# Kernel tuning notes

Measured on AMD Instinct MI355X. Metric: run time of the kernel, lower is better.

The kernel has to match this reference:

```python
import jax, jax.numpy as jnp
import numpy as np
from jax import lax

B, S, D, H = 8, 1024, 512, 8
K = 25  # moving-average kernel
EPS = 1e-6


def setup_inputs() -> dict:
    key = jax.random.key(0)
    ks = jax.random.split(key, 8)

    def dense_w(k, din, dout):
        return (jax.random.normal(k, (din, dout), jnp.float32) / np.sqrt(din).astype(np.float32))

    return {
        "x": jax.random.normal(ks[0], (B, S, D), jnp.float32),
        "wq": dense_w(ks[1], D, D), "bq": jnp.zeros((D,), jnp.float32),
        "wk": dense_w(ks[2], D, D), "bk": jnp.zeros((D,), jnp.float32),
        "wv": dense_w(ks[3], D, D), "bv": jnp.zeros((D,), jnp.float32),
        "wo": dense_w(ks[4], D, D), "bo": jnp.zeros((D,), jnp.float32),
        "w1": dense_w(ks[5], D, 4 * D), "b1": jnp.zeros((4 * D,), jnp.float32),
        "w2": dense_w(ks[6], 4 * D, D), "b2": jnp.zeros((D,), jnp.float32),
        "g1": jnp.ones((D,), jnp.float32), "be1": jnp.zeros((D,), jnp.float32),
        "g2": jnp.ones((D,), jnp.float32), "be2": jnp.zeros((D,), jnp.float32),
        "g3": jnp.ones((D,), jnp.float32), "be3": jnp.zeros((D,), jnp.float32),
        "num_heads": H,
    }


def _moving_avg(x):
    # TF AveragePooling1D(pool=K, stride=1, padding='same'): divisor excludes padding.
    s = lax.reduce_window(x, 0.0, lax.add, (1, K, 1), (1, 1, 1), 'SAME')
    cnt = lax.reduce_window(jnp.ones((1, x.shape[1], 1), x.dtype), 0.0, lax.add,
                            (1, K, 1), (1, 1, 1), 'SAME')
    return s / cnt


def _layernorm(x, g, b):
    m = jnp.mean(x, -1, keepdims=True)
    v = jnp.var(x, -1, keepdims=True)
    return (x - m) * jax.lax.rsqrt(v + EPS) * g + b


def _auto_correlation(x, wq, bq, wk, bk, wv, bv, wo, bo, num_heads):
    b, s, d = x.shape
    dp = d // num_heads
    def split_heads(t):
        return t.reshape(b, s, num_heads, dp).transpose(0, 2, 1, 3)  # [B,H,S,dp]
    q = split_heads(x @ wq + bq)
    k = split_heads(x @ wk + bk)
    v = split_heads(x @ wv + bv)
    # Faithful to source: rfft over innermost (depth) axis, fft_length = 2*S.
    qf = jnp.fft.rfft(q, n=2 * s, axis=-1)
    kf = jnp.fft.rfft(k, n=2 * s, axis=-1)
    corr = jnp.fft.irfft(qf * jnp.conj(kf), n=2 * s, axis=-1)[..., :s]  # [B,H,S,S]
    scale = 1.0 / np.sqrt(dp).astype(np.float32)
    attn = jax.nn.softmax(scale * corr, axis=-1)
    out = jnp.einsum('bhst,bhtd->bhsd', attn, v)
    out = out.transpose(0, 2, 1, 3).reshape(b, s, d)
    return out @ wo + bo


def reference(x, wq, bq, wk, bk, wv, bv, wo, bo, w1, b1, w2, b2,
              g1, be1, g2, be2, g3, be3, num_heads):
    trend_init = _moving_avg(x)
    seasonal_init = x - trend_init
    attn_out = _auto_correlation(seasonal_init, wq, bq, wk, bk, wv, bv, wo, bo, num_heads)
    out1 = _layernorm(attn_out + seasonal_init, g1, be1)
    ffn = jax.nn.relu(out1 @ w1 + b1) @ w2 + b2
    seasonal_out = _layernorm(out1 + ffn, g2, be2) + seasonal_init
    trend2 = _moving_avg(seasonal_out)
    seasonal_final = seasonal_out - trend2
    x_out = seasonal_final + (trend2 + trend_init)
    return _layernorm(x_out, g3, be3)
```

## Files before the change

### kernel.cpp

```cpp
#include <hip/hip_runtime.h>
#include <cstdint>


typedef float f32x4 __attribute__((ext_vector_type(4)));
typedef __bf16 bf16x8 __attribute__((ext_vector_type(8)));
typedef _Float16 h2t __attribute__((ext_vector_type(2)));
typedef unsigned short u16;
typedef unsigned int u32;
typedef u32 u32x4 __attribute__((ext_vector_type(4)));

__device__ __forceinline__ u16 f2bf(float f) {
  unsigned int u = __float_as_uint(f);
  u = (u + 0x7FFFu + ((u >> 16) & 1u)) >> 16;
  return (u16)u;
}

__device__ __forceinline__ float bf2f(u16 b) { return __uint_as_float((u32)b << 16); }

__device__ __forceinline__ u16 f2h(float f) {
  _Float16 hv = (_Float16)f;
  u16 b;
  __builtin_memcpy(&b, &hv, 2);
  return b;
}

__device__ __forceinline__ float dot2h(u32 qp, u32 kp_, float c) {
#if __has_builtin(__builtin_amdgcn_fdot2)
  return __builtin_amdgcn_fdot2(__builtin_bit_cast(h2t, qp),
                                __builtin_bit_cast(h2t, kp_), c, false);
#else
  h2t q = __builtin_bit_cast(h2t, qp), k = __builtin_bit_cast(h2t, kp_);
  c = fmaf((float)q.x, (float)k.x, c);
  return fmaf((float)q.y, (float)k.y, c);
#endif
}

__device__ __forceinline__ void gload_lds16(const void* g, void* l) {
  __builtin_amdgcn_global_load_lds((__attribute__((address_space(1))) void*)g,
                                   (__attribute__((address_space(3))) void*)l,
                                   16, 0, 0);
}

__global__ __launch_bounds__(256) void movavg_kernel(
    const float* __restrict__ x, float* __restrict__ seas,
    u16* __restrict__ seas_bf, u16* __restrict__ a64, float* __restrict__ srow) {
  int blk = blockIdx.x;
  int sc = blk & 127, b = blk >> 7;
  int d = threadIdx.x * 2;
  const float* xb = x + (size_t)b * 1024 * 512 + d;
  int s0 = sc * 8;
  int lo = max(s0 - 12, 0), hi = min(s0 + 12, 1023);
  float sx = 0.f, sy = 0.f;
  for (int j = lo; j <= hi; ++j) {
    float2 v = *(const float2*)&xb[(size_t)j * 512];
    sx += v.x;
    sy += v.y;
  }
  float ax = 0.f, ay = 0.f;
#pragma unroll
  for (int s = s0; s < s0 + 8; ++s) {
    int l2 = max(s - 12, 0), h2 = min(s + 12, 1023);
    float invc = 1.f / (float)(h2 - l2 + 1);
    float2 xv = *(const float2*)&xb[(size_t)s * 512];
    float sex = xv.x - sx * invc;
    float sey = xv.y - sy * invc;
    size_t idx = (size_t)(b * 1024 + s) * 512 + d;
    u32 pk = (u32)f2bf(sex) | ((u32)f2bf(sey) << 16);
    *(float2*)&seas[idx] = make_float2(sex, sey);
    *(u32*)&seas_bf[idx] = pk;
    if (s < 64) *(u32*)&a64[(size_t)(b * 64 + s) * 512 + d] = pk;
    ax += sex;
    ay += sey;
    if (s - 12 >= 0) {
      float2 v = *(const float2*)&xb[(size_t)(s - 12) * 512];
      sx -= v.x;
      sy -= v.y;
    }
    if (s + 13 <= 1023) {
      float2 v = *(const float2*)&xb[(size_t)(s + 13) * 512];
      sx += v.x;
      sy += v.y;
    }
  }
  atomicAdd(&srow[b * 512 + d], ax);
  atomicAdd(&srow[b * 512 + d + 1], ay);
}

__global__ __launch_bounds__(256) void weights_prep_kernel(
    const float* __restrict__ wq, const float* __restrict__ wk,
    const float* __restrict__ wv, const float* __restrict__ wo,
    const float* __restrict__ w1, const float* __restrict__ w2,
    const float* __restrict__ bq, const float* __restrict__ bk,
    u16* __restrict__ wqkt, u16* __restrict__ wvt, u16* __restrict__ wot,
    u16* __restrict__ w1t, u16* __restrict__ w2t, float* __restrict__ qkbias) {
  __shared__ float tile[32][33];
  int i = blockIdx.x;
  int tx = threadIdx.x, ty = threadIdx.y;
  if (i >= 3072) {
    int idx = (i - 3072) * 256 + ty * 32 + tx;
    qkbias[idx] = idx < 512 ? bq[idx] : bk[idx - 512];
    return;
  }
  const float* src;
  u16* dst;
  int R, C, bx, by;
  if (i < 1024) {
    int w = i >> 8, l = i & 255;
    src = (w == 0 ? wq : w == 1 ? wk : w == 2 ? wv : wo);
    dst = (w == 0 ? wqkt : w == 1 ? wqkt + 512 * 512 : w == 2 ? wvt : wot);
    R = 512; C = 512; bx = l & 15; by = l >> 4;
  } else if (i < 2048) {
    int l = i - 1024;
    src = w1; dst = w1t; R = 512; C = 2048; bx = l & 15; by = l >> 4;
  } else {
    int l = i - 2048;
    src = w2; dst = w2t; R = 2048; C = 512; bx = l & 63; by = l >> 6;
  }
  int r0 = bx * 32, c0 = by * 32;
#pragma unroll
  for (int k = 0; k < 4; ++k)
    tile[ty + 8 * k][tx] = src[(size_t)(r0 + ty + 8 * k) * C + c0 + tx];
  __syncthreads();
#pragma unroll
  for (int k = 0; k < 4; ++k)
    dst[(size_t)(c0 + ty + 8 * k) * R + r0 + tx] = f2bf(tile[tx][ty + 8 * k]);
}

__global__ __launch_bounds__(256) void vsum_kernel(
    const float* __restrict__ srow, const float* __restrict__ wv,
    const float* __restrict__ bv, float* __restrict__ vsum) {
  int blk = blockIdx.x;
  int b = blk >> 1;
  int n = (blk & 1) * 256 + threadIdx.x;
  float acc = 0.f;
  for (int k = 0; k < 512; ++k) acc += srow[b * 512 + k] * wv[(size_t)k * 512 + n];
  vsum[b * 512 + n] = acc + 1024.f * bv[n];
}

template <int RELU, int OMODE, int KSPLIT>
__global__ __launch_bounds__(256, 4) void gemm_bf16_kernel(
    const u16* __restrict__ A, const u16* __restrict__ Bt,
    const float* __restrict__ bias, void* __restrict__ Cv, void* __restrict__ Cv2,
    int M, int N, int K) {
  constexpr int BK = 32;
  __shared__ u16 As[3][128 * BK];
  __shared__ u16 Bs[3][64 * BK];
  const int tid = threadIdx.x;
  const int wid = tid >> 6, lane = tid & 63;
  const int wm = wid >> 1, wn = wid & 1;
  const int la = lane & 15, lg = lane >> 4;
  int nwg = gridDim.x * gridDim.y;
  int lin = blockIdx.y * gridDim.x + blockIdx.x;
  int swz = (lin & 7) * (nwg >> 3) + (lin >> 3);
  int bx = swz / gridDim.y;
  int by = swz % gridDim.y;
  const int row0 = bx * 128, col0 = by * 64;
  const int z = (KSPLIT > 1) ? (int)blockIdx.z : 0;
  const int kbeg = z * (K / KSPLIT);
  const int ksteps = (K / KSPLIT) / BK;
  f32x4 acc[4][2] = {};

  auto stage = [&](int buf, int k0) {
    {
      int p = tid, r = p >> 2, cg = (p & 3) ^ ((r >> 1) & 3);
      gload_lds16(A + (size_t)(row0 + r) * K + k0 + cg * 8, ((char*)As[buf]) + p * 16);
    }
    {
      int p = tid + 256, r = p >> 2, cg = (p & 3) ^ ((r >> 1) & 3);
      gload_lds16(A + (size_t)(row0 + r) * K + k0 + cg * 8, ((char*)As[buf]) + p * 16);
    }
    {
      int p = tid, r = p >> 2, cg = (p & 3) ^ ((r >> 1) & 3);
      gload_lds16(Bt + (size_t)(col0 + r) * K + k0 + cg * 8, ((char*)Bs[buf]) + p * 16);
    }
  };

  stage(0, kbeg);
  stage(1, kbeg + BK);
  asm volatile("s_waitcnt vmcnt(3)" ::: "memory");
  __builtin_amdgcn_s_barrier();
  __builtin_amdgcn_sched_barrier(0);

  for (int t = 0; t < ksteps; ++t) {
    const int cur = t % 3;
    if (t + 2 < ksteps) stage((t + 2) % 3, kbeg + (t + 2) * BK);
    __builtin_amdgcn_sched_barrier(0);
    bf16x8 af[4], bfr[2];
#pragma unroll
    for (int m = 0; m < 4; ++m) {
      int r = wm * 64 + m * 16 + la;
      int cp = lg ^ ((r >> 1) & 3);
      af[m] = *(const bf16x8*)(((const char*)As[cur]) + r * 64 + cp * 16);
    }
#pragma unroll
    for (int n = 0; n < 2; ++n) {
      int r = wn * 32 + n * 16 + la;
      int cp = lg ^ ((r >> 1) & 3);
      bfr[n] = *(const bf16x8*)(((const char*)Bs[cur]) + r * 64 + cp * 16);
    }
    __builtin_amdgcn_s_setprio(1);
#pragma unroll
    for (int m = 0; m < 4; ++m)
#pragma unroll
      for (int n = 0; n < 2; ++n)
        acc[m][n] = __builtin_amdgcn_mfma_f32_16x16x32_bf16(af[m], bfr[n], acc[m][n], 0, 0, 0);
    __builtin_amdgcn_s_setprio(0);
    if (t + 2 < ksteps)
      asm volatile("s_waitcnt vmcnt(3)" ::: "memory");
    else
      asm volatile("s_waitcnt vmcnt(0)" ::: "memory");
    __builtin_amdgcn_s_barrier();
    __builtin_amdgcn_sched_barrier(0);
  }

  void* Cout = (z == 0) ? Cv : Cv2;
#pragma unroll
  for (int m = 0; m < 4; ++m) {
    int r = row0 + wm * 64 + m * 16 + lg * 4;
#pragma unroll
    for (int n = 0; n < 2; ++n) {
      int cc = col0 + wn * 32 + n * 16 + la;
      float bvv = (z == 0) ? bias[cc] : 0.f;
#pragma unroll
      for (int j = 0; j < 4; ++j) {
        float v = acc[m][n][j] + bvv;
        if (RELU) v = fmaxf(v, 0.f);
        if constexpr (OMODE == 0) {
          ((float*)Cout)[(size_t)(r + j) * N + cc] = v;
        } else if constexpr (OMODE == 1) {
          ((u16*)Cout)[(size_t)(r + j) * N + cc] = f2bf(v);
        } else if constexpr (OMODE == 2) {
          ((u16*)Cout)[(size_t)(r + j) * N + cc] = f2h(v);
        } else {
          int rr = r + j;
          int bb = rr >> 6, tt = rr & 63, hh = cc >> 6, dd = cc & 63;
          ((u16*)Cout)[(((size_t)bb * 8 + hh) * 64 + dd) * 64 + tt] = f2bf(v);
        }
      }
    }
  }
}

__global__ __launch_bounds__(256) void attn_mfma_kernel(
    const u16* __restrict__ qk, const u16* __restrict__ v64t,
    const float* __restrict__ vsum, u16* __restrict__ attn_bf) {
  __shared__ u32 qE[32][64];
  __shared__ u32 qO[32][64];
  __shared__ u32 kp[32][32];
  __shared__ u16 coef[32][64];
  __shared__ u16 vtt[64][64];
  __shared__ float zc[32];
  __shared__ float Vs[64];
  int bid = blockIdx.x;
  int scnk = bid & 31, h = (bid >> 5) & 7, b = bid >> 8;
  int tid = threadIdx.x, wid = tid >> 6, lane = tid & 63;
  int bh = b * 8 + h;

  {
    int p = tid, r = p >> 3, cc = p & 7;
    gload_lds16(v64t + ((size_t)bh * 4096 + r * 64 + ((cc ^ (r & 7)) * 8)),
                ((char*)vtt) + p * 16);
    p = tid + 256; r = p >> 3; cc = p & 7;
    gload_lds16(v64t + ((size_t)bh * 4096 + r * 64 + ((cc ^ (r & 7)) * 8)),
                ((char*)vtt) + p * 16);
  }
  *(f32x4*)&qE[tid >> 3][32 + ((tid & 7) << 2)] = f32x4{};
  {
    int s = tid >> 3, c = tid & 7;
    size_t grow = ((size_t)(b * 1024 + scnk * 32 + s)) * 1024 + h * 64;
    *(f32x4*)&qE[s][c * 4] = *(const f32x4*)&qk[grow + c * 8];
    *(f32x4*)&kp[s][c * 4] = *(const f32x4*)&qk[grow + 512 + c * 8];
  }
  if (tid < 64) Vs[tid] = vsum[b * 512 + h * 64 + tid];
  __syncthreads();
  for (int j2 = tid; j2 < 1024; j2 += 256) {
    int s = j2 >> 5, j = j2 & 31;
    u32 a = qE[s][j], b2 = qE[s][j + 1];
    qO[s][j] = (a >> 16) | (b2 << 16);
    qO[s][j + 32] = 0;
  }
  __syncthreads();
  for (int i = 0; i < 8; ++i) {
    int s = wid * 8 + i;
    u32x4 kk4[8];
#pragma unroll
    for (int u = 0; u < 8; ++u) kk4[u] = *(const u32x4*)&kp[s][u * 4];
    int t = lane, sel = t & 1;
    const u32* qptr = (sel ? qO[s] : qE[s]) + (t >> 1);
    float c = 0.f;
#pragma unroll
    for (int u = 0; u < 8; ++u) {
#pragma unroll
      for (int v = 0; v < 4; ++v) c = dot2h(qptr[u * 4 + v], kk4[u][v], c);
    }
    float sc = c * 0.125f;
    float mx = fmaxf(sc, 0.f);
#pragma unroll
    for (int off = 32; off >= 1; off >>= 1) mx = fmaxf(mx, __shfl_xor(mx, off));
    float w = __expf(sc - mx), wz = __expf(-mx);
    float sw = w;
#pragma unroll
    for (int off = 32; off >= 1; off >>= 1) sw += __shfl_xor(sw, off);
    float inv = 1.f / (sw + 960.f * wz);
    *(u16*)(((char*)&coef[s][0]) + ((2 * t) ^ ((s & 7) << 4))) = f2bf((w - wz) * inv);
    if (lane == 0) zc[s] = wz * inv;
  }
  __syncthreads();
  {
    int sm = wid >> 1, nh = wid & 1;
    int la = lane & 15, lg = lane >> 4;
    int r = sm * 16 + la;
    int n0 = nh * 32 + la, n1 = nh * 32 + 16 + la;
    f32x4 acc0 = {}, acc1 = {};
#pragma unroll
    for (int ks = 0; ks < 2; ++ks) {
      int lr = ks * 4 + lg;
      bf16x8 af = *(const bf16x8*)(((const char*)coef) + r * 128 + ((lr ^ (r & 7)) << 4));
      bf16x8 bf0 = *(const bf16x8*)(((const char*)vtt) + n0 * 128 + ((lr ^ (n0 & 7)) << 4));
      bf16x8 bf1 = *(const bf16x8*)(((const char*)vtt) + n1 * 128 + ((lr ^ (n1 & 7)) << 4));
      acc0 = __builtin_amdgcn_mfma_f32_16x16x32_bf16(af, bf0, acc0, 0, 0, 0);
      acc1 = __builtin_amdgcn_mfma_f32_16x16x32_bf16(af, bf1, acc1, 0, 0, 0);
    }
    int srl0 = sm * 16 + lg * 4;
    int srow0 = b * 1024 + scnk * 32 + srl0;
    float vs0 = Vs[nh * 32 + la], vs1 = Vs[nh * 32 + 16 + la];
#pragma unroll
    for (int j = 0; j < 4; ++j) {
      float zcv = zc[srl0 + j];
      size_t rb = (size_t)(srow0 + j) * 512 + h * 64;
      attn_bf[rb + nh * 32 + la] = f2bf(acc0[j] + zcv * vs0);
      attn_bf[rb + nh * 32 + 16 + la] = f2bf(acc1[j] + zcv * vs1);
    }
  }
}

__device__ __forceinline__ void block_reduce_2(float& a, float& b, float* sbuf) {
  int tid = threadIdx.x, wid = tid >> 6, lane = tid & 63;
#pragma unroll
  for (int off = 32; off >= 1; off >>= 1) {
    a += __shfl_xor(a, off);
    b += __shfl_xor(b, off);
  }
  if (lane == 0) {
    sbuf[wid] = a;
    sbuf[4 + wid] = b;
  }
  __syncthreads();
  a = sbuf[0] + sbuf[1] + sbuf[2] + sbuf[3];
  b = sbuf[4] + sbuf[5] + sbuf[6] + sbuf[7];
  __syncthreads();
}

__global__ __launch_bounds__(256) void ln_res_kernel(
    const u16* __restrict__ xa, const u16* __restrict__ xb,
    const float* __restrict__ res,
    const float* __restrict__ g, const float* __restrict__ be,
    float* __restrict__ outf, u16* __restrict__ outbf) {
  __shared__ float sbuf[8];
  int row = blockIdx.x, tid = threadIdx.x;
  int d = tid * 2;
  size_t base = (size_t)row * 512 + d;
  u32 pa = *(const u32*)&xa[base];
  u32 pb = *(const u32*)&xb[base];
  float2 r = *(const float2*)&res[base];
  float v0 = bf2f((u16)pa) + bf2f((u16)pb) + r.x;
  float v1 = bf2f((u16)(pa >> 16)) + bf2f((u16)(pb >> 16)) + r.y;
  float s = v0 + v1, q = v0 * v0 + v1 * v1;
  block_reduce_2(s, q, sbuf);
  float mean = s * (1.f / 512.f);
  float var = q * (1.f / 512.f) - mean * mean;
  float rs = rsqrtf(var + 1e-6f);
  float2 gg = *(const float2*)&g[d];
  float2 bb = *(const float2*)&be[d];
  float o0 = (v0 - mean) * rs * gg.x + bb.x;
  float o1 = (v1 - mean) * rs * gg.y + bb.y;
  *(float2*)&outf[base] = make_float2(o0, o1);
  *(u32*)&outbf[base] = (u32)f2bf(o0) | ((u32)f2bf(o1) << 16);
}

__global__ __launch_bounds__(256) void final_kernel(
    const float* __restrict__ out1, const u16* __restrict__ fa,
    const u16* __restrict__ fb, const float* __restrict__ x,
    const float* __restrict__ g2, const float* __restrict__ be2,
    const float* __restrict__ g3, const float* __restrict__ be3,
    float* __restrict__ out) {
  __shared__ float sbuf[8];
  int row = blockIdx.x, tid = threadIdx.x;
  int d = tid * 2;
  size_t base = (size_t)row * 512 + d;
  float2 a = *(const float2*)&out1[base];
  u32 pa = *(const u32*)&fa[base];
  u32 pb = *(const u32*)&fb[base];
  float t0 = a.x + bf2f((u16)pa) + bf2f((u16)pb);
  float t1 = a.y + bf2f((u16)(pa >> 16)) + bf2f((u16)(pb >> 16));
  float s = t0 + t1, q = t0 * t0 + t1 * t1;
  block_reduce_2(s, q, sbuf);
  float mean = s * (1.f / 512.f);
  float var = q * (1.f / 512.f) - mean * mean;
  float rs = rsqrtf(var + 1e-6f);
  float2 g2v = *(const float2*)&g2[d];
  float2 b2v = *(const float2*)&be2[d];
  float2 xv = *(const float2*)&x[base];
  float y0 = (t0 - mean) * rs * g2v.x + b2v.x + xv.x;
  float y1 = (t1 - mean) * rs * g2v.y + b2v.y + xv.y;
  s = y0 + y1;
  q = y0 * y0 + y1 * y1;
  block_reduce_2(s, q, sbuf);
  mean = s * (1.f / 512.f);
  var = q * (1.f / 512.f) - mean * mean;
  rs = rsqrtf(var + 1e-6f);
  float2 g3v = *(const float2*)&g3[d];
  float2 b3v = *(const float2*)&be3[d];
  float2 o = make_float2((y0 - mean) * rs * g3v.x + b3v.x,
                         (y1 - mean) * rs * g3v.y + b3v.y);
  *(float2*)&out[base] = o;
}

extern "C" void kernel_launch(void* const* d_in, const int* in_sizes, int n_in,
                              void* d_out, int out_size, void* d_ws, size_t ws_size,
                              hipStream_t stream) {
  const float* x = (const float*)d_in[0];
  const float* wq = (const float*)d_in[1];
  const float* bq = (const float*)d_in[2];
  const float* wk = (const float*)d_in[3];
  const float* bk = (const float*)d_in[4];
  const float* wv = (const float*)d_in[5];
  const float* bv = (const float*)d_in[6];
  const float* wo = (const float*)d_in[7];
  const float* bo = (const float*)d_in[8];
  const float* w1 = (const float*)d_in[9];
  const float* b1 = (const float*)d_in[10];
  const float* w2 = (const float*)d_in[11];
  const float* b2 = (const float*)d_in[12];
  const float* g1 = (const float*)d_in[13];
  const float* be1 = (const float*)d_in[14];
  const float* g2 = (const float*)d_in[15];
  const float* be2 = (const float*)d_in[16];
  const float* g3 = (const float*)d_in[17];
  const float* be3 = (const float*)d_in[18];
  float* out = (float*)d_out;

  const size_t MS = 8192ull * 512ull;
  float* seasonal = (float*)d_ws;
  float* out1 = seasonal + MS;
  float* projf = out1 + MS;
  float* srow = projf + MS;
  float* vsumb = srow + 4096;
  float* qkbias = vsumb + 4096;
  u16* qk_f16 = (u16*)(qkbias + 1024);
  u16* hidden = qk_f16 + 8192ull * 1024;
  u16* seas_bf = hidden + 8192ull * 2048;
  u16* attn_bf = seas_bf + MS;
  u16* v64t = attn_bf + MS;
  u16* a64_bf = v64t + 512 * 512;
  u16* wqkt = a64_bf + 512 * 512;
  u16* wvt = wqkt + 1024 * 512;
  u16* wot = wvt + 512 * 512;
  u16* w1t = wot + 512 * 512;
  u16* w2t = w1t + 2048ull * 512;
  u16* wo0 = (u16*)projf;
  u16* wo1 = wo0 + MS;
  u16* ff0 = qk_f16;
  u16* ff1 = ff0 + MS;

  hipMemsetAsync(srow, 0, 4096 * sizeof(float), stream);
  weights_prep_kernel<<<3076, dim3(32, 8), 0, stream>>>(
      wq, wk, wv, wo, w1, w2, bq, bk, wqkt, wvt, wot, w1t, w2t, qkbias);

  movavg_kernel<<<1024, 256, 0, stream>>>(x, seasonal, seas_bf, a64_bf, srow);
  vsum_kernel<<<16, 256, 0, stream>>>(srow, wv, bv, vsumb);

  gemm_bf16_kernel<0, 2, 1><<<dim3(64, 16), 256, 0, stream>>>(
      seas_bf, wqkt, qkbias, qk_f16, nullptr, 8192, 1024, 512);
  gemm_bf16_kernel<0, 3, 1><<<dim3(4, 8), 256, 0, stream>>>(
      a64_bf, wvt, bv, v64t, nullptr, 512, 512, 512);

  attn_mfma_kernel<<<2048, 256, 0, stream>>>(qk_f16, v64t, vsumb, attn_bf);

  gemm_bf16_kernel<0, 1, 2><<<dim3(64, 8, 2), 256, 0, stream>>>(
      attn_bf, wot, bo, wo0, wo1, 8192, 512, 512);
  ln_res_kernel<<<8192, 256, 0, stream>>>(wo0, wo1, seasonal, g1, be1, out1, seas_bf);

  gemm_bf16_kernel<1, 1, 1><<<dim3(64, 32), 256, 0, stream>>>(
      seas_bf, w1t, b1, hidden, nullptr, 8192, 2048, 512);
  gemm_bf16_kernel<0, 1, 2><<<dim3(64, 8, 2), 256, 0, stream>>>(
      hidden, w2t, b2, ff0, ff1, 8192, 512, 2048);

  final_kernel<<<8192, 256, 0, stream>>>(out1, ff0, ff1, x, g2, be2, g3, be3, out);
}
```

Baseline: 223.4 us.

## Drop fp32 intermediates for bf16 residuals and deepen GEMM pipeline to four stages

The seasonal and out1 fp32 buffers are removed. The residual into the first layernorm now reads the bf16 seasonal copy, and out1 is stored only in bf16 in place, which cuts global memory traffic in the elementwise kernels. Separately, the GEMM moves from a 3-stage to a 4-stage LDS prefetch pipeline, with occupancy lowered to 3 blocks per SM to hide load latency. The cost is lower precision on the residual paths, and the extra LDS per block reduces occupancy.

```diff
diff --git a/kernel.cpp b/kernel.cpp
--- a/kernel.cpp
+++ b/kernel.cpp
@@ -42,8 +42,8 @@
 }
 
 __global__ __launch_bounds__(256) void movavg_kernel(
-    const float* __restrict__ x, float* __restrict__ seas,
-    u16* __restrict__ seas_bf, u16* __restrict__ a64, float* __restrict__ srow) {
+    const float* __restrict__ x, u16* __restrict__ seas_bf,
+    u16* __restrict__ a64, float* __restrict__ srow) {
   int blk = blockIdx.x;
   int sc = blk & 127, b = blk >> 7;
   int d = threadIdx.x * 2;
@@ -66,7 +66,6 @@
     float sey = xv.y - sy * invc;
     size_t idx = (size_t)(b * 1024 + s) * 512 + d;
     u32 pk = (u32)f2bf(sex) | ((u32)f2bf(sey) << 16);
-    *(float2*)&seas[idx] = make_float2(sex, sey);
     *(u32*)&seas_bf[idx] = pk;
     if (s < 64) *(u32*)&a64[(size_t)(b * 64 + s) * 512 + d] = pk;
     ax += sex;
@@ -138,13 +137,13 @@
 }
 
 template <int RELU, int OMODE, int KSPLIT>
-__global__ __launch_bounds__(256, 4) void gemm_bf16_kernel(
+__global__ __launch_bounds__(256, 3) void gemm_bf16_kernel(
     const u16* __restrict__ A, const u16* __restrict__ Bt,
     const float* __restrict__ bias, void* __restrict__ Cv, void* __restrict__ Cv2,
     int M, int N, int K) {
   constexpr int BK = 32;
-  __shared__ u16 As[3][128 * BK];
-  __shared__ u16 Bs[3][64 * BK];
+  __shared__ u16 As[4][128 * BK];
+  __shared__ u16 Bs[4][64 * BK];
   const int tid = threadIdx.x;
   const int wid = tid >> 6, lane = tid & 63;
   const int wm = wid >> 1, wn = wid & 1;
@@ -177,13 +176,14 @@
 
   stage(0, kbeg);
   stage(1, kbeg + BK);
-  asm volatile("s_waitcnt vmcnt(3)" ::: "memory");
+  stage(2, kbeg + 2 * BK);
+  asm volatile("s_waitcnt vmcnt(6)" ::: "memory");
   __builtin_amdgcn_s_barrier();
   __builtin_amdgcn_sched_barrier(0);
 
   for (int t = 0; t < ksteps; ++t) {
-    const int cur = t % 3;
-    if (t + 2 < ksteps) stage((t + 2) % 3, kbeg + (t + 2) * BK);
+    const int cur = t & 3;
+    if (t + 3 < ksteps) stage((t + 3) & 3, kbeg + (t + 3) * BK);
     __builtin_amdgcn_sched_barrier(0);
     bf16x8 af[4], bfr[2];
 #pragma unroll
@@ -205,7 +205,9 @@
       for (int n = 0; n < 2; ++n)
         acc[m][n] = __builtin_amdgcn_mfma_f32_16x16x32_bf16(af[m], bfr[n], acc[m][n], 0, 0, 0);
     __builtin_amdgcn_s_setprio(0);
-    if (t + 2 < ksteps)
+    if (t + 3 < ksteps)
+      asm volatile("s_waitcnt vmcnt(6)" ::: "memory");
+    else if (t + 2 < ksteps)
       asm volatile("s_waitcnt vmcnt(3)" ::: "memory");
     else
       asm volatile("s_waitcnt vmcnt(0)" ::: "memory");
@@ -353,18 +355,17 @@
 
 __global__ __launch_bounds__(256) void ln_res_kernel(
     const u16* __restrict__ xa, const u16* __restrict__ xb,
-    const float* __restrict__ res,
-    const float* __restrict__ g, const float* __restrict__ be,
-    float* __restrict__ outf, u16* __restrict__ outbf) {
+    u16* __restrict__ res_out,
+    const float* __restrict__ g, const float* __restrict__ be) {
   __shared__ float sbuf[8];
   int row = blockIdx.x, tid = threadIdx.x;
   int d = tid * 2;
   size_t base = (size_t)row * 512 + d;
   u32 pa = *(const u32*)&xa[base];
   u32 pb = *(const u32*)&xb[base];
-  float2 r = *(const float2*)&res[base];
-  float v0 = bf2f((u16)pa) + bf2f((u16)pb) + r.x;
-  float v1 = bf2f((u16)(pa >> 16)) + bf2f((u16)(pb >> 16)) + r.y;
+  u32 pr = *(const u32*)&res_out[base];
+  float v0 = bf2f((u16)pa) + bf2f((u16)pb) + bf2f((u16)pr);
+  float v1 = bf2f((u16)(pa >> 16)) + bf2f((u16)(pb >> 16)) + bf2f((u16)(pr >> 16));
   float s = v0 + v1, q = v0 * v0 + v1 * v1;
   block_reduce_2(s, q, sbuf);
   float mean = s * (1.f / 512.f);
@@ -374,12 +375,11 @@
   float2 bb = *(const float2*)&be[d];
   float o0 = (v0 - mean) * rs * gg.x + bb.x;
   float o1 = (v1 - mean) * rs * gg.y + bb.y;
-  *(float2*)&outf[base] = make_float2(o0, o1);
-  *(u32*)&outbf[base] = (u32)f2bf(o0) | ((u32)f2bf(o1) << 16);
+  *(u32*)&res_out[base] = (u32)f2bf(o0) | ((u32)f2bf(o1) << 16);
 }
 
 __global__ __launch_bounds__(256) void final_kernel(
-    const float* __restrict__ out1, const u16* __restrict__ fa,
+    const u16* __restrict__ out1, const u16* __restrict__ fa,
     const u16* __restrict__ fb, const float* __restrict__ x,
     const float* __restrict__ g2, const float* __restrict__ be2,
     const float* __restrict__ g3, const float* __restrict__ be3,
@@ -388,11 +388,11 @@
   int row = blockIdx.x, tid = threadIdx.x;
   int d = tid * 2;
   size_t base = (size_t)row * 512 + d;
-  float2 a = *(const float2*)&out1[base];
+  u32 po = *(const u32*)&out1[base];
   u32 pa = *(const u32*)&fa[base];
   u32 pb = *(const u32*)&fb[base];
-  float t0 = a.x + bf2f((u16)pa) + bf2f((u16)pb);
-  float t1 = a.y + bf2f((u16)(pa >> 16)) + bf2f((u16)(pb >> 16));
+  float t0 = bf2f((u16)po) + bf2f((u16)pa) + bf2f((u16)pb);
+  float t1 = bf2f((u16)(po >> 16)) + bf2f((u16)(pa >> 16)) + bf2f((u16)(pb >> 16));
   float s = t0 + t1, q = t0 * t0 + t1 * t1;
   block_reduce_2(s, q, sbuf);
   float mean = s * (1.f / 512.f);
@@ -441,25 +441,22 @@
   float* out = (float*)d_out;
 
   const size_t MS = 8192ull * 512ull;
-  float* seasonal = (float*)d_ws;
-  float* out1 = seasonal + MS;
-  float* projf = out1 + MS;
-  float* srow = projf + MS;
+  float* srow = (float*)d_ws;
   float* vsumb = srow + 4096;
   float* qkbias = vsumb + 4096;
   u16* qk_f16 = (u16*)(qkbias + 1024);
   u16* hidden = qk_f16 + 8192ull * 1024;
   u16* seas_bf = hidden + 8192ull * 2048;
   u16* attn_bf = seas_bf + MS;
-  u16* v64t = attn_bf + MS;
+  u16* wo0 = attn_bf + MS;
+  u16* wo1 = wo0 + MS;
+  u16* v64t = wo1 + MS;
   u16* a64_bf = v64t + 512 * 512;
   u16* wqkt = a64_bf + 512 * 512;
   u16* wvt = wqkt + 1024 * 512;
   u16* wot = wvt + 512 * 512;
   u16* w1t = wot + 512 * 512;
   u16* w2t = w1t + 2048ull * 512;
-  u16* wo0 = (u16*)projf;
-  u16* wo1 = wo0 + MS;
   u16* ff0 = qk_f16;
   u16* ff1 = ff0 + MS;
 
@@ -467,7 +464,7 @@
   weights_prep_kernel<<<3076, dim3(32, 8), 0, stream>>>(
       wq, wk, wv, wo, w1, w2, bq, bk, wqkt, wvt, wot, w1t, w2t, qkbias);
 
-  movavg_kernel<<<1024, 256, 0, stream>>>(x, seasonal, seas_bf, a64_bf, srow);
+  movavg_kernel<<<1024, 256, 0, stream>>>(x, seas_bf, a64_bf, srow);
   vsum_kernel<<<16, 256, 0, stream>>>(srow, wv, bv, vsumb);
 
   gemm_bf16_kernel<0, 2, 1><<<dim3(64, 16), 256, 0, stream>>>(
@@ -479,12 +476,12 @@
 
   gemm_bf16_kernel<0, 1, 2><<<dim3(64, 8, 2), 256, 0, stream>>>(
       attn_bf, wot, bo, wo0, wo1, 8192, 512, 512);
-  ln_res_kernel<<<8192, 256, 0, stream>>>(wo0, wo1, seasonal, g1, be1, out1, seas_bf);
+  ln_res_kernel<<<8192, 256, 0, stream>>>(wo0, wo1, seas_bf, g1, be1);
 
   gemm_bf16_kernel<1, 1, 1><<<dim3(64, 32), 256, 0, stream>>>(
       seas_bf, w1t, b1, hidden, nullptr, 8192, 2048, 512);
   gemm_bf16_kernel<0, 1, 2><<<dim3(64, 8, 2), 256, 0, stream>>>(
       hidden, w2t, b2, ff0, ff1, 8192, 512, 2048);
 
-  final_kernel<<<8192, 256, 0, stream>>>(out1, ff0, ff1, x, g2, be2, g3, be3, out);
-}
+  final_kernel<<<8192, 256, 0, stream>>>(seas_bf, ff0, ff1, x, g2, be2, g3, be3, out);
+}
```

Measured after the change: 236.4 us. +5.8%, slower.
